# Kernel optimization log

Measured on AMD Instinct MI355X. Metric: run time of the kernel, lower is better.

Reference implementation:

```python
import jax, jax.numpy as jnp
import numpy as np

B, S, D, H = 2, 2048, 1024, 16
DH = D // H
EPS = 1e-5
NEG = -1e9


def layer_norm(x, scale, bias):
    mu = jnp.mean(x, axis=-1, keepdims=True)
    var = jnp.mean((x - mu) ** 2, axis=-1, keepdims=True)
    return (x - mu) * jax.lax.rsqrt(var + EPS) * scale + bias


def setup_inputs() -> dict:
    key = jax.random.key(0)
    ks = jax.random.split(key, 8)
    scale = 1.0 / np.sqrt(D)
    x = jax.random.normal(ks[0], (B, S, D), dtype=jnp.float32)
    padding_mask = jnp.ones((B, S), dtype=bool)
    # per-head QKV projections stacked over heads: (H, D, DH)
    Wq = jax.random.normal(ks[1], (H, D, DH), dtype=jnp.float32) * scale
    Wk = jax.random.normal(ks[2], (H, D, DH), dtype=jnp.float32) * scale
    Wv = jax.random.normal(ks[3], (H, D, DH), dtype=jnp.float32) * scale
    ln1_s = jnp.ones((D,), jnp.float32); ln1_b = jnp.zeros((D,), jnp.float32)
    ln2_s = jnp.ones((D,), jnp.float32); ln2_b = jnp.zeros((D,), jnp.float32)
    W1 = jax.random.normal(ks[4], (D, D), dtype=jnp.float32) * scale
    b1 = jnp.zeros((D,), jnp.float32)
    W2 = jax.random.normal(ks[5], (D, D), dtype=jnp.float32) * scale
    b2 = jnp.zeros((D,), jnp.float32)
    return dict(x=x, padding_mask=padding_mask, Wq=Wq, Wk=Wk, Wv=Wv,
                ln1_s=ln1_s, ln1_b=ln1_b, ln2_s=ln2_s, ln2_b=ln2_b,
                W1=W1, b1=b1, W2=W2, b2=b2)


def reference(x, padding_mask, Wq, Wk, Wv, ln1_s, ln1_b, ln2_s, ln2_b, W1, b1, W2, b2):
    # pre-norm attention with residual (dropout = identity at eval)
    h = layer_norm(x, ln1_s, ln1_b)
    q = jnp.einsum('bsd,hde->bhse', h, Wq)
    k = jnp.einsum('bsd,hde->bhse', h, Wk)
    v = jnp.einsum('bsd,hde->bhse', h, Wv)
    scores = jnp.einsum('bhse,bhte->bhst', q, k) / jnp.sqrt(jnp.float32(DH))
    causal = jnp.tril(jnp.ones((S, S), dtype=bool))           # (S,S)
    mask = padding_mask[:, None, None, :] & causal[None, None]  # (B,1,S,S)
    scores = jnp.where(mask, scores, NEG)
    p = jax.nn.softmax(scores, axis=-1)
    z = jnp.einsum('bhst,bhte->bshe', p, v).reshape(x.shape[0], x.shape[1], D)
    x = x + z
    # pre-norm FFN with residual
    h2 = layer_norm(x, ln2_s, ln2_b)
    ff = jax.nn.relu(h2 @ W1 + b1) @ W2 + b2
    return x + ff
```

## Files before the change

### kernel.cpp

```cpp
#include <hip/hip_runtime.h>
#include <hip/hip_bf16.h>
#include <stdint.h>

#define NB 2
#define NS 2048
#define ND 1024
#define NH 16
#define NDH 64
#define NT (NB*NS)

using f32x4  = __attribute__((ext_vector_type(4))) float;
using bf16x8 = __attribute__((ext_vector_type(8))) short;

typedef __attribute__((address_space(1))) unsigned int as1_uint;
typedef __attribute__((address_space(3))) unsigned int as3_uint;

#if __has_builtin(__builtin_amdgcn_exp2f)
#define EXP2 __builtin_amdgcn_exp2f
#else
#define EXP2 exp2f
#endif

__device__ __forceinline__ void llds16(void* l, const void* g) {
    __builtin_amdgcn_global_load_lds((as1_uint*)g, (as3_uint*)l, 16, 0, 0);
}

__device__ __forceinline__ f32x4 mfma16(bf16x8 a, bf16x8 b, f32x4 c) {
    return __builtin_amdgcn_mfma_f32_16x16x32_bf16(a, b, c, 0, 0, 0);
}

__device__ __forceinline__ unsigned short f2bf(float f) {
    union { __hip_bfloat16 h; unsigned short u; } cv;
    cv.h = __float2bfloat16(f);
    return cv.u;
}

__global__ void k_prep_ln(const float* __restrict__ Wq, const float* __restrict__ Wk,
                          const float* __restrict__ Wv, const float* __restrict__ W1,
                          const float* __restrict__ W2, unsigned short* __restrict__ WcatT,
                          unsigned short* __restrict__ W1T, unsigned short* __restrict__ W2T,
                          const float* __restrict__ x, const float* __restrict__ sc,
                          const float* __restrict__ bi, unsigned short* __restrict__ hout) {
    __shared__ float tile[64][65];
    __shared__ float ssum[4], ssq[4];
    int tid = threadIdx.x;
    int bid = blockIdx.x;
    if (bid < 768) {
        const float SCALEQ = 0.125f * 1.44269504088896f;
        int kt = bid & 15; bid >>= 4;
        int h  = bid & 15; bid >>= 4;
        int mat = bid;
        const float* W = (mat == 0) ? Wq : (mat == 1) ? Wk : Wv;
#pragma unroll
        for (int i = 0; i < 16; ++i) {
            int idx = tid + i * 256;
            int r = idx >> 6, e = idx & 63;
            tile[r][e] = W[(size_t)h * ND * NDH + (size_t)(kt * 64 + r) * NDH + e];
        }
        __syncthreads();
#pragma unroll
        for (int i = 0; i < 16; ++i) {
            int idx = tid + i * 256;
            int e = idx >> 6, r = idx & 63;
            float v = tile[r][e];
            if (mat == 0) v *= SCALEQ;
            WcatT[(size_t)(mat * 1024 + h * 64 + e) * ND + kt * 64 + r] = f2bf(v);
        }
    } else if (bid < 1280) {
        const float* W = (bid < 1024) ? W1 : W2;
        unsigned short* WT = (bid < 1024) ? W1T : W2T;
        int lb = (bid - 768) & 255;
        int ntile = lb & 15;
        int ktile = lb >> 4;
#pragma unroll
        for (int i = 0; i < 16; ++i) {
            int idx = tid + i * 256;
            int r = idx >> 6, c = idx & 63;
            tile[r][c] = W[(size_t)(ktile * 64 + r) * ND + ntile * 64 + c];
        }
        __syncthreads();
#pragma unroll
        for (int i = 0; i < 16; ++i) {
            int idx = tid + i * 256;
            int c = idx >> 6, r = idx & 63;
            WT[(size_t)(ntile * 64 + c) * ND + ktile * 64 + r] = f2bf(tile[r][c]);
        }
    } else {
        int row = bid - 1280;
        const float* xr = x + (size_t)row * ND;
        float4 v = reinterpret_cast<const float4*>(xr)[tid];
        float sum = v.x + v.y + v.z + v.w;
        float sq  = v.x * v.x + v.y * v.y + v.z * v.z + v.w * v.w;
#pragma unroll
        for (int off = 1; off < 64; off <<= 1) {
            sum += __shfl_xor(sum, off);
            sq  += __shfl_xor(sq, off);
        }
        int wave = tid >> 6;
        if ((tid & 63) == 0) { ssum[wave] = sum; ssq[wave] = sq; }
        __syncthreads();
        sum = ssum[0] + ssum[1] + ssum[2] + ssum[3];
        sq  = ssq[0] + ssq[1] + ssq[2] + ssq[3];
        float mu  = sum * (1.0f / ND);
        float var = sq * (1.0f / ND) - mu * mu;
        float rstd = rsqrtf(var + 1e-5f);
        float4 s4 = reinterpret_cast<const float4*>(sc)[tid];
        float4 b4 = reinterpret_cast<const float4*>(bi)[tid];
        ushort4 o;
        o.x = f2bf((v.x - mu) * rstd * s4.x + b4.x);
        o.y = f2bf((v.y - mu) * rstd * s4.y + b4.y);
        o.z = f2bf((v.z - mu) * rstd * s4.z + b4.z);
        o.w = f2bf((v.w - mu) * rstd * s4.w + b4.w);
        reinterpret_cast<ushort4*>(hout + (size_t)row * ND)[tid] = o;
    }
}

__global__ void k_ln(const float* __restrict__ x, const float* __restrict__ sc,
                     const float* __restrict__ bi, unsigned short* __restrict__ out) {
    int row = blockIdx.x;
    int tid = threadIdx.x;
    const float* xr = x + (size_t)row * ND;
    float4 v = reinterpret_cast<const float4*>(xr)[tid];
    float sum = v.x + v.y + v.z + v.w;
    float sq  = v.x * v.x + v.y * v.y + v.z * v.z + v.w * v.w;
#pragma unroll
    for (int off = 1; off < 64; off <<= 1) {
        sum += __shfl_xor(sum, off);
        sq  += __shfl_xor(sq, off);
    }
    __shared__ float ssum[4], ssq[4];
    int wave = tid >> 6;
    if ((tid & 63) == 0) { ssum[wave] = sum; ssq[wave] = sq; }
    __syncthreads();
    sum = ssum[0] + ssum[1] + ssum[2] + ssum[3];
    sq  = ssq[0] + ssq[1] + ssq[2] + ssq[3];
    float mu  = sum * (1.0f / ND);
    float var = sq * (1.0f / ND) - mu * mu;
    float rstd = rsqrtf(var + 1e-5f);
    float4 s4 = reinterpret_cast<const float4*>(sc)[tid];
    float4 b4 = reinterpret_cast<const float4*>(bi)[tid];
    ushort4 o;
    o.x = f2bf((v.x - mu) * rstd * s4.x + b4.x);
    o.y = f2bf((v.y - mu) * rstd * s4.y + b4.y);
    o.z = f2bf((v.z - mu) * rstd * s4.z + b4.z);
    o.w = f2bf((v.w - mu) * rstd * s4.w + b4.w);
    reinterpret_cast<ushort4*>(out + (size_t)row * ND)[tid] = o;
}

template<bool BIAS, bool RELU, bool RES>
__device__ __forceinline__
void gemm_core(const unsigned short* __restrict__ A, const unsigned short* __restrict__ Bt,
               const float* __restrict__ bias, const float* __restrict__ res,
               void* __restrict__ Cv, int N, int K, int wg) {
    __shared__ __align__(16) unsigned short As[2][64 * 64];
    __shared__ __align__(16) unsigned short Bs[2][128 * 64];
    int tid = threadIdx.x;
    int lane = tid & 63, wave = tid >> 6;
    int wm = wave >> 1, wn = wave & 1;
    int l16 = lane & 15, lg = lane >> 4;
    int ntiles = N >> 7;
    int mt = wg / ntiles;
    int nt = wg % ntiles;

    const unsigned short* Abase = A  + (size_t)(mt * 64) * K;
    const unsigned short* Bbase = Bt + (size_t)(nt * 128) * K;

    f32x4 acc[2][4];
#pragma unroll
    for (int i = 0; i < 2; ++i)
#pragma unroll
        for (int j = 0; j < 4; ++j) acc[i][j] = (f32x4){0.f, 0.f, 0.f, 0.f};

    int srow = tid >> 3;
    int sch  = tid & 7;
    int KT = K >> 6;

    auto STAGE = [&](int kt, int bufi) {
#pragma unroll
        for (int i = 0; i < 2; ++i) {
            int row = srow + i * 32;
            int cs = sch ^ (row & 7);
            llds16((char*)As[bufi] + wave * 1024 + i * 4096,
                   Abase + (size_t)row * K + kt * 64 + cs * 8);
        }
#pragma unroll
        for (int i = 0; i < 4; ++i) {
            int row = srow + i * 32;
            int cs = sch ^ (row & 7);
            llds16((char*)Bs[bufi] + wave * 1024 + i * 4096,
                   Bbase + (size_t)row * K + kt * 64 + cs * 8);
        }
    };

    STAGE(0, 0);
    for (int kt = 0; kt < KT; ++kt) {
        int cb = kt & 1;
        if (kt + 1 < KT) {
            STAGE(kt + 1, cb ^ 1);
            asm volatile("s_waitcnt vmcnt(6)" ::: "memory");
        } else {
            asm volatile("s_waitcnt vmcnt(0)" ::: "memory");
        }
        __builtin_amdgcn_s_barrier();

        bf16x8 af[2][2], bfb[4][2];
#pragma unroll
        for (int mi = 0; mi < 2; ++mi)
#pragma unroll
            for (int kc = 0; kc < 2; ++kc) {
                int row = wm * 32 + mi * 16 + l16;
                int ch = (kc * 4 + lg) ^ (row & 7);
                af[mi][kc] = *reinterpret_cast<const bf16x8*>((const char*)As[cb] + row * 128 + ch * 16);
            }
#pragma unroll
        for (int ni = 0; ni < 4; ++ni)
#pragma unroll
            for (int kc = 0; kc < 2; ++kc) {
                int row = wn * 64 + ni * 16 + l16;
                int ch = (kc * 4 + lg) ^ (row & 7);
                bfb[ni][kc] = *reinterpret_cast<const bf16x8*>((const char*)Bs[cb] + row * 128 + ch * 16);
            }
#pragma unroll
        for (int mi = 0; mi < 2; ++mi)
#pragma unroll
            for (int ni = 0; ni < 4; ++ni) {
                acc[mi][ni] = mfma16(af[mi][0], bfb[ni][0], acc[mi][ni]);
                acc[mi][ni] = mfma16(af[mi][1], bfb[ni][1], acc[mi][ni]);
            }
        __builtin_amdgcn_s_barrier();
    }

#pragma unroll
    for (int mi = 0; mi < 2; ++mi)
#pragma unroll
        for (int ni = 0; ni < 4; ++ni) {
            int col = nt * 128 + wn * 64 + ni * 16 + l16;
            float bv = BIAS ? bias[col] : 0.f;
#pragma unroll
            for (int r = 0; r < 4; ++r) {
                int row = mt * 64 + wm * 32 + mi * 16 + lg * 4 + r;
                float v = acc[mi][ni][r] + bv;
                if (RELU) v = fmaxf(v, 0.f);
                size_t idx = (size_t)row * N + col;
                if (RES) ((float*)Cv)[idx] = v + res[idx];
                else ((unsigned short*)Cv)[idx] = f2bf(v);
            }
        }
}

template<bool BIAS, bool RELU, bool RES>
__global__ __launch_bounds__(256)
void k_gemm(const unsigned short* __restrict__ A, const unsigned short* __restrict__ Bt,
            const float* __restrict__ bias, const float* __restrict__ res,
            void* __restrict__ Cv, int N, int K) {
    int wg = (blockIdx.x & 7) * (gridDim.x >> 3) + (blockIdx.x >> 3);
    gemm_core<BIAS, RELU, RES>(A, Bt, bias, res, Cv, N, K, wg);
}

__global__ __launch_bounds__(256)
void k_gemm_dual(const unsigned short* __restrict__ A0, const unsigned short* __restrict__ Bt0,
                 void* __restrict__ C0, int N0,
                 const unsigned short* __restrict__ A1, const unsigned short* __restrict__ Bt1,
                 void* __restrict__ C1, int N1, int K, int split) {
    int bid = blockIdx.x;
    if (bid < split) {
        int wg = (bid & 7) * (split >> 3) + (bid >> 3);
        gemm_core<false, false, false>(A0, Bt0, nullptr, nullptr, C0, N0, K, wg);
    } else {
        int lb = bid - split;
        int nblk = gridDim.x - split;
        int wg = (lb & 7) * (nblk >> 3) + (lb >> 3);
        gemm_core<false, false, false>(A1, Bt1, nullptr, nullptr, C1, N1, K, wg);
    }
}

__global__ __launch_bounds__(256)
void k_attn(const unsigned short* __restrict__ qk, const unsigned short* __restrict__ VT,
            const float* __restrict__ x, float* __restrict__ x2) {
    constexpr int ldq = 2 * ND;
    int bid = blockIdx.x;
    int c  = bid & 255;
    int g  = bid >> 8;
    int s  = c >> 5;
    int bh = c & 31;
    int qb = (g == 0) ? 31 - s : (g == 1) ? 16 + s : (g == 2) ? 15 - s : s;
    int h = bh & 15, b = bh >> 4;
    int tid = threadIdx.x;
    int lane = tid & 63, wave = tid >> 6;
    int l16 = lane & 15, lg = lane >> 4;

    const unsigned short* Qp = qk + (size_t)b * NS * ldq + h * NDH;
    const unsigned short* Kp = Qp + ND;
    const unsigned short* Vp = VT + (size_t)(h * NDH) * NT + b * NS;

    __shared__ __align__(16) unsigned short Ks[2][64 * 64];
    __shared__ __align__(16) unsigned short Vs[2][64 * 64];
    __shared__ __align__(16) unsigned short Ps[4][16 * 64];

    int srow = tid >> 3;
    int sch  = tid & 7;
    int scs  = sch ^ (srow & 7);

    int nt = qb + 1;
    int qw = qb * 64 + wave * 16;

    const unsigned short* Kst = Kp + (size_t)srow * ldq + scs * 8;
    const unsigned short* Vst = Vp + (size_t)srow * NT + scs * 8;

    bf16x8 qf[2];
#pragma unroll
    for (int kc = 0; kc < 2; ++kc)
        qf[kc] = *reinterpret_cast<const bf16x8*>(Qp + (size_t)(qw + l16) * ldq + kc * 32 + lg * 8);

    bf16x8 vone;
#pragma unroll
    for (int i = 0; i < 8; ++i) vone[i] = (short)0x3F80;

    f32x4 oacc[4];
#pragma unroll
    for (int i = 0; i < 4; ++i) oacc[i] = (f32x4){0.f, 0.f, 0.f, 0.f};
    f32x4 lacc = (f32x4){0.f, 0.f, 0.f, 0.f};

    char* pbase = (char*)&Ps[wave][0] + l16 * 128;
    int psw = l16 & 7;

    llds16((char*)Ks[0] + wave * 1024,        Kst);
    llds16((char*)Ks[0] + wave * 1024 + 4096, Kst + (size_t)32 * ldq);
    llds16((char*)Vs[0] + wave * 1024,        Vst);
    llds16((char*)Vs[0] + wave * 1024 + 4096, Vst + (size_t)32 * NT);
    const unsigned short* Kn = Kst + (size_t)64 * ldq;
    const unsigned short* Vn = Vst + 64;

    for (int t = 0; t < nt; ++t) {
        int cur = t & 1;
        const char* Kcur = (const char*)Ks[cur];
        const char* Vcur = (const char*)Vs[cur];

        if (t + 1 < nt) {
            char* kd = (char*)Ks[cur ^ 1] + wave * 1024;
            char* vd = (char*)Vs[cur ^ 1] + wave * 1024;
            llds16(kd,        Kn);
            llds16(kd + 4096, Kn + (size_t)32 * ldq);
            llds16(vd,        Vn);
            llds16(vd + 4096, Vn + (size_t)32 * NT);
            Kn += (size_t)64 * ldq;
            Vn += 64;
            asm volatile("s_waitcnt vmcnt(4)" ::: "memory");
        } else {
            asm volatile("s_waitcnt vmcnt(0)" ::: "memory");
        }
        __builtin_amdgcn_s_barrier();

        f32x4 st[4];
#pragma unroll
        for (int mtt = 0; mtt < 4; ++mtt) st[mtt] = (f32x4){0.f, 0.f, 0.f, 0.f};
        __builtin_amdgcn_s_setprio(1);
#pragma unroll
        for (int kc = 0; kc < 2; ++kc)
#pragma unroll
            for (int mtt = 0; mtt < 4; ++mtt) {
                int row = mtt * 16 + l16;
                int ch = (kc * 4 + lg) ^ (row & 7);
                bf16x8 kf = *reinterpret_cast<const bf16x8*>(Kcur + row * 128 + ch * 16);
                st[mtt] = mfma16(kf, qf[kc], st[mtt]);
            }
        __builtin_amdgcn_s_setprio(0);

        if (t == qb) {
            int qg = qw + l16;
#pragma unroll
            for (int mtt = 0; mtt < 4; ++mtt)
#pragma unroll
                for (int r = 0; r < 4; ++r) {
                    int key = t * 64 + mtt * 16 + lg * 4 + r;
                    st[mtt][r] = (key <= qg) ? st[mtt][r] : -1.0e30f;
                }
        }
#pragma unroll
        for (int mtt = 0; mtt < 4; ++mtt) {
            float p0 = EXP2(st[mtt][0]);
            float p1 = EXP2(st[mtt][1]);
            float p2 = EXP2(st[mtt][2]);
            float p3 = EXP2(st[mtt][3]);
            int b0 = mtt * 32 + lg * 8;
            int sb = ((((b0 >> 4) ^ psw) << 4) | (b0 & 15));
            uint2 u;
            u.x = (unsigned)f2bf(p0) | ((unsigned)f2bf(p1) << 16);
            u.y = (unsigned)f2bf(p2) | ((unsigned)f2bf(p3) << 16);
            *reinterpret_cast<uint2*>(pbase + sb) = u;
        }

        asm volatile("s_waitcnt lgkmcnt(0)" ::: "memory");

        __builtin_amdgcn_s_setprio(1);
#pragma unroll
        for (int kc = 0; kc < 2; ++kc) {
            bf16x8 pa = *reinterpret_cast<const bf16x8*>(pbase + (((kc * 4 + lg) ^ psw) << 4));
            lacc = mfma16(pa, vone, lacc);
#pragma unroll
            for (int ntt = 0; ntt < 4; ++ntt) {
                int vrow = ntt * 16 + l16;
                bf16x8 vb = *reinterpret_cast<const bf16x8*>(
                    Vcur + vrow * 128 + ((((kc * 4 + lg) ^ (vrow & 7)) << 4)));
                oacc[ntt] = mfma16(pa, vb, oacc[ntt]);
            }
        }
        __builtin_amdgcn_s_setprio(0);
        __builtin_amdgcn_s_barrier();
    }

#pragma unroll
    for (int r = 0; r < 4; ++r) {
        float linv = 1.0f / lacc[r];
        int tkn = b * NS + qw + lg * 4 + r;
        size_t base = (size_t)tkn * ND + h * NDH;
#pragma unroll
        for (int ntt = 0; ntt < 4; ++ntt) {
            size_t idx = base + ntt * 16 + l16;
            x2[idx] = x[idx] + oacc[ntt][r] * linv;
        }
    }
}

extern "C" void kernel_launch(void* const* d_in, const int* in_sizes, int n_in,
                              void* d_out, int out_size, void* d_ws, size_t ws_size,
                              hipStream_t stream) {
    const float* x    = (const float*)d_in[0];
    const float* Wq   = (const float*)d_in[2];
    const float* Wk   = (const float*)d_in[3];
    const float* Wv   = (const float*)d_in[4];
    const float* ln1s = (const float*)d_in[5];
    const float* ln1b = (const float*)d_in[6];
    const float* ln2s = (const float*)d_in[7];
    const float* ln2b = (const float*)d_in[8];
    const float* W1   = (const float*)d_in[9];
    const float* b1   = (const float*)d_in[10];
    const float* W2   = (const float*)d_in[11];
    const float* b2   = (const float*)d_in[12];
    float* out = (float*)d_out;

    char* ws = (char*)d_ws;
    unsigned short* WcatT = (unsigned short*)(ws);
    unsigned short* W1T   = (unsigned short*)(ws + 6291456);
    unsigned short* W2T   = (unsigned short*)(ws + 8388608);
    unsigned short* hbuf  = (unsigned short*)(ws + 10485760);
    unsigned short* qkbuf = (unsigned short*)(ws + 18874368);
    unsigned short* vtbuf = (unsigned short*)(ws + 35651584);
    float*          x2    = (float*)(ws + 44040192);
    unsigned short* ubuf  = qkbuf;

    k_prep_ln<<<1280 + NT, 256, 0, stream>>>(Wq, Wk, Wv, W1, W2, WcatT, W1T, W2T,
                                             x, ln1s, ln1b, hbuf);
    k_gemm_dual<<<1024 + 512, 256, 0, stream>>>(
        hbuf, WcatT, qkbuf, 2048,
        WcatT + (size_t)2048 * 1024, hbuf, vtbuf, NT, 1024, 1024);
    k_attn<<<NB * NH * 32, 256, 0, stream>>>(qkbuf, vtbuf, x, x2);
    k_ln<<<NT, 256, 0, stream>>>(x2, ln2s, ln2b, hbuf);
    k_gemm<true, true, false><<<(NT / 64) * (1024 / 128), 256, 0, stream>>>(
        hbuf, W1T, b1, nullptr, ubuf, 1024, 1024);
    k_gemm<true, false, true><<<(NT / 64) * (1024 / 128), 256, 0, stream>>>(
        ubuf, W2T, b2, x2, out, 1024, 1024);
}
```

Measured before the change: 129.7 us.

## Split causal attention KV range across two blocks and fuse merge into LN2

Each query block's causal key range is split into two halves processed by separate workgroups, doubling the grid to 2048 blocks for better load balance and occupancy. Each half writes unnormalized bf16 partial outputs and row sums. A new combine+layernorm kernel merges the halves, adds the residual, writes x2 into the output buffer, and produces the LN2 input, replacing the separate LN kernel. Partial outputs are rounded to bf16 before normalization, which adds rounding error. The merge skips max rescaling, so it relies on the scores never needing a running max.

```diff
diff --git a/kernel.cpp b/kernel.cpp
--- a/kernel.cpp
+++ b/kernel.cpp
@@ -33,6 +33,10 @@
     union { __hip_bfloat16 h; unsigned short u; } cv;
     cv.h = __float2bfloat16(f);
     return cv.u;
+}
+
+__device__ __forceinline__ float bf2f(unsigned short u) {
+    return __uint_as_float((unsigned)u << 16);
 }
 
 __global__ void k_prep_ln(const float* __restrict__ Wq, const float* __restrict__ Wk,
@@ -115,12 +119,314 @@
     }
 }
 
-__global__ void k_ln(const float* __restrict__ x, const float* __restrict__ sc,
-                     const float* __restrict__ bi, unsigned short* __restrict__ out) {
+template<bool BIAS, bool RELU, bool RES>
+__device__ __forceinline__
+void gemm_core(const unsigned short* __restrict__ A, const unsigned short* __restrict__ Bt,
+               const float* __restrict__ bias, const float* __restrict__ res,
+               void* __restrict__ Cv, int N, int K, int wg) {
+    __shared__ __align__(16) unsigned short As[2][64 * 64];
+    __shared__ __align__(16) unsigned short Bs[2][128 * 64];
+    int tid = threadIdx.x;
+    int lane = tid & 63, wave = tid >> 6;
+    int wm = wave >> 1, wn = wave & 1;
+    int l16 = lane & 15, lg = lane >> 4;
+    int ntiles = N >> 7;
+    int mt = wg / ntiles;
+    int nt = wg % ntiles;
+
+    const unsigned short* Abase = A  + (size_t)(mt * 64) * K;
+    const unsigned short* Bbase = Bt + (size_t)(nt * 128) * K;
+
+    f32x4 acc[2][4];
+#pragma unroll
+    for (int i = 0; i < 2; ++i)
+#pragma unroll
+        for (int j = 0; j < 4; ++j) acc[i][j] = (f32x4){0.f, 0.f, 0.f, 0.f};
+
+    int srow = tid >> 3;
+    int sch  = tid & 7;
+    int KT = K >> 6;
+
+    auto STAGE = [&](int kt, int bufi) {
+#pragma unroll
+        for (int i = 0; i < 2; ++i) {
+            int row = srow + i * 32;
+            int cs = sch ^ (row & 7);
+            llds16((char*)As[bufi] + wave * 1024 + i * 4096,
+                   Abase + (size_t)row * K + kt * 64 + cs * 8);
+        }
+#pragma unroll
+        for (int i = 0; i < 4; ++i) {
+            int row = srow + i * 32;
+            int cs = sch ^ (row & 7);
+            llds16((char*)Bs[bufi] + wave * 1024 + i * 4096,
+                   Bbase + (size_t)row * K + kt * 64 + cs * 8);
+        }
+    };
+
+    STAGE(0, 0);
+    for (int kt = 0; kt < KT; ++kt) {
+        int cb = kt & 1;
+        if (kt + 1 < KT) {
+            STAGE(kt + 1, cb ^ 1);
+            asm volatile("s_waitcnt vmcnt(6)" ::: "memory");
+        } else {
+            asm volatile("s_waitcnt vmcnt(0)" ::: "memory");
+        }
+        __builtin_amdgcn_s_barrier();
+
+        bf16x8 af[2][2], bfb[4][2];
+#pragma unroll
+        for (int mi = 0; mi < 2; ++mi)
+#pragma unroll
+            for (int kc = 0; kc < 2; ++kc) {
+                int row = wm * 32 + mi * 16 + l16;
+                int ch = (kc * 4 + lg) ^ (row & 7);
+                af[mi][kc] = *reinterpret_cast<const bf16x8*>((const char*)As[cb] + row * 128 + ch * 16);
+            }
+#pragma unroll
+        for (int ni = 0; ni < 4; ++ni)
+#pragma unroll
+            for (int kc = 0; kc < 2; ++kc) {
+                int row = wn * 64 + ni * 16 + l16;
+                int ch = (kc * 4 + lg) ^ (row & 7);
+                bfb[ni][kc] = *reinterpret_cast<const bf16x8*>((const char*)Bs[cb] + row * 128 + ch * 16);
+            }
+#pragma unroll
+        for (int mi = 0; mi < 2; ++mi)
+#pragma unroll
+            for (int ni = 0; ni < 4; ++ni) {
+                acc[mi][ni] = mfma16(af[mi][0], bfb[ni][0], acc[mi][ni]);
+                acc[mi][ni] = mfma16(af[mi][1], bfb[ni][1], acc[mi][ni]);
+            }
+        __builtin_amdgcn_s_barrier();
+    }
+
+#pragma unroll
+    for (int mi = 0; mi < 2; ++mi)
+#pragma unroll
+        for (int ni = 0; ni < 4; ++ni) {
+            int col = nt * 128 + wn * 64 + ni * 16 + l16;
+            float bv = BIAS ? bias[col] : 0.f;
+#pragma unroll
+            for (int r = 0; r < 4; ++r) {
+                int row = mt * 64 + wm * 32 + mi * 16 + lg * 4 + r;
+                float v = acc[mi][ni][r] + bv;
+                if (RELU) v = fmaxf(v, 0.f);
+                size_t idx = (size_t)row * N + col;
+                if (RES) ((float*)Cv)[idx] = v + res[idx];
+                else ((unsigned short*)Cv)[idx] = f2bf(v);
+            }
+        }
+}
+
+template<bool BIAS, bool RELU, bool RES>
+__global__ __launch_bounds__(256)
+void k_gemm(const unsigned short* __restrict__ A, const unsigned short* __restrict__ Bt,
+            const float* __restrict__ bias, const float* __restrict__ res,
+            void* __restrict__ Cv, int N, int K) {
+    int wg = (blockIdx.x & 7) * (gridDim.x >> 3) + (blockIdx.x >> 3);
+    gemm_core<BIAS, RELU, RES>(A, Bt, bias, res, Cv, N, K, wg);
+}
+
+__global__ __launch_bounds__(256)
+void k_gemm_dual(const unsigned short* __restrict__ A0, const unsigned short* __restrict__ Bt0,
+                 void* __restrict__ C0, int N0,
+                 const unsigned short* __restrict__ A1, const unsigned short* __restrict__ Bt1,
+                 void* __restrict__ C1, int N1, int K, int split) {
+    int bid = blockIdx.x;
+    if (bid < split) {
+        int wg = (bid & 7) * (split >> 3) + (bid >> 3);
+        gemm_core<false, false, false>(A0, Bt0, nullptr, nullptr, C0, N0, K, wg);
+    } else {
+        int lb = bid - split;
+        int nblk = gridDim.x - split;
+        int wg = (lb & 7) * (nblk >> 3) + (lb >> 3);
+        gemm_core<false, false, false>(A1, Bt1, nullptr, nullptr, C1, N1, K, wg);
+    }
+}
+
+__global__ __launch_bounds__(256)
+void k_attn(const unsigned short* __restrict__ qk, const unsigned short* __restrict__ VT,
+            unsigned short* __restrict__ Oa, unsigned short* __restrict__ Ob,
+            float* __restrict__ lp) {
+    constexpr int ldq = 2 * ND;
+    int bid = blockIdx.x;
+    int bh = bid & 31;
+    int j  = bid >> 5;
+    int qb = 31 - (j >> 1);
+    int half = j & 1;
+    int h = bh & 15, b = bh >> 4;
+    int tid = threadIdx.x;
+    int lane = tid & 63, wave = tid >> 6;
+    int l16 = lane & 15, lg = lane >> 4;
+
+    const unsigned short* Qp = qk + (size_t)b * NS * ldq + h * NDH;
+    const unsigned short* Kp = Qp + ND;
+    const unsigned short* Vp = VT + (size_t)(h * NDH) * NT + b * NS;
+
+    __shared__ __align__(16) unsigned short Ks[2][64 * 64];
+    __shared__ __align__(16) unsigned short Vs[2][64 * 64];
+    __shared__ __align__(16) unsigned short Ps[4][16 * 64];
+
+    int srow = tid >> 3;
+    int sch  = tid & 7;
+    int scs  = sch ^ (srow & 7);
+
+    int ntA = (qb + 2) >> 1;
+    int t0 = half ? ntA : 0;
+    int t1 = half ? (qb + 1) : ntA;
+    int ntiles = t1 - t0;
+    int qw = qb * 64 + wave * 16;
+
+    const unsigned short* Kst = Kp + (size_t)srow * ldq + scs * 8 + (size_t)t0 * 64 * ldq;
+    const unsigned short* Vst = Vp + (size_t)srow * NT + scs * 8 + t0 * 64;
+
+    bf16x8 qf[2];
+#pragma unroll
+    for (int kc = 0; kc < 2; ++kc)
+        qf[kc] = *reinterpret_cast<const bf16x8*>(Qp + (size_t)(qw + l16) * ldq + kc * 32 + lg * 8);
+
+    bf16x8 vone;
+#pragma unroll
+    for (int i = 0; i < 8; ++i) vone[i] = (short)0x3F80;
+
+    f32x4 oacc[4];
+#pragma unroll
+    for (int i = 0; i < 4; ++i) oacc[i] = (f32x4){0.f, 0.f, 0.f, 0.f};
+    f32x4 lacc = (f32x4){0.f, 0.f, 0.f, 0.f};
+
+    char* pbase = (char*)&Ps[wave][0] + l16 * 128;
+    int psw = l16 & 7;
+
+    if (ntiles > 0) {
+        llds16((char*)Ks[0] + wave * 1024,        Kst);
+        llds16((char*)Ks[0] + wave * 1024 + 4096, Kst + (size_t)32 * ldq);
+        llds16((char*)Vs[0] + wave * 1024,        Vst);
+        llds16((char*)Vs[0] + wave * 1024 + 4096, Vst + (size_t)32 * NT);
+    }
+    const unsigned short* Kn = Kst + (size_t)64 * ldq;
+    const unsigned short* Vn = Vst + 64;
+
+    for (int i = 0; i < ntiles; ++i) {
+        int cur = i & 1;
+        int t = t0 + i;
+        const char* Kcur = (const char*)Ks[cur];
+        const char* Vcur = (const char*)Vs[cur];
+
+        if (i + 1 < ntiles) {
+            char* kd = (char*)Ks[cur ^ 1] + wave * 1024;
+            char* vd = (char*)Vs[cur ^ 1] + wave * 1024;
+            llds16(kd,        Kn);
+            llds16(kd + 4096, Kn + (size_t)32 * ldq);
+            llds16(vd,        Vn);
+            llds16(vd + 4096, Vn + (size_t)32 * NT);
+            Kn += (size_t)64 * ldq;
+            Vn += 64;
+            asm volatile("s_waitcnt vmcnt(4)" ::: "memory");
+        } else {
+            asm volatile("s_waitcnt vmcnt(0)" ::: "memory");
+        }
+        __builtin_amdgcn_s_barrier();
+
+        f32x4 st[4];
+#pragma unroll
+        for (int mtt = 0; mtt < 4; ++mtt) st[mtt] = (f32x4){0.f, 0.f, 0.f, 0.f};
+        __builtin_amdgcn_s_setprio(1);
+#pragma unroll
+        for (int kc = 0; kc < 2; ++kc)
+#pragma unroll
+            for (int mtt = 0; mtt < 4; ++mtt) {
+                int row = mtt * 16 + l16;
+                int ch = (kc * 4 + lg) ^ (row & 7);
+                bf16x8 kf = *reinterpret_cast<const bf16x8*>(Kcur + row * 128 + ch * 16);
+                st[mtt] = mfma16(kf, qf[kc], st[mtt]);
+            }
+        __builtin_amdgcn_s_setprio(0);
+
+        if (t == qb) {
+            int qg = qw + l16;
+#pragma unroll
+            for (int mtt = 0; mtt < 4; ++mtt)
+#pragma unroll
+                for (int r = 0; r < 4; ++r) {
+                    int key = t * 64 + mtt * 16 + lg * 4 + r;
+                    st[mtt][r] = (key <= qg) ? st[mtt][r] : -1.0e30f;
+                }
+        }
+#pragma unroll
+        for (int mtt = 0; mtt < 4; ++mtt) {
+            float p0 = EXP2(st[mtt][0]);
+            float p1 = EXP2(st[mtt][1]);
+            float p2 = EXP2(st[mtt][2]);
+            float p3 = EXP2(st[mtt][3]);
+            int b0 = mtt * 32 + lg * 8;
+            int sb = ((((b0 >> 4) ^ psw) << 4) | (b0 & 15));
+            uint2 u;
+            u.x = (unsigned)f2bf(p0) | ((unsigned)f2bf(p1) << 16);
+            u.y = (unsigned)f2bf(p2) | ((unsigned)f2bf(p3) << 16);
+            *reinterpret_cast<uint2*>(pbase + sb) = u;
+        }
+
+        asm volatile("s_waitcnt lgkmcnt(0)" ::: "memory");
+
+        __builtin_amdgcn_s_setprio(1);
+#pragma unroll
+        for (int kc = 0; kc < 2; ++kc) {
+            bf16x8 pa = *reinterpret_cast<const bf16x8*>(pbase + (((kc * 4 + lg) ^ psw) << 4));
+            lacc = mfma16(pa, vone, lacc);
+#pragma unroll
+            for (int ntt = 0; ntt < 4; ++ntt) {
+                int vrow = ntt * 16 + l16;
+                bf16x8 vb = *reinterpret_cast<const bf16x8*>(
+                    Vcur + vrow * 128 + ((((kc * 4 + lg) ^ (vrow & 7)) << 4)));
+                oacc[ntt] = mfma16(pa, vb, oacc[ntt]);
+            }
+        }
+        __builtin_amdgcn_s_setprio(0);
+        __builtin_amdgcn_s_barrier();
+    }
+
+    unsigned short* Op = half ? Ob : Oa;
+#pragma unroll
+    for (int r = 0; r < 4; ++r) {
+        int tkn = b * NS + qw + lg * 4 + r;
+        size_t base = (size_t)tkn * ND + h * NDH;
+#pragma unroll
+        for (int ntt = 0; ntt < 4; ++ntt)
+            Op[base + ntt * 16 + l16] = f2bf(oacc[ntt][r]);
+    }
+    if (l16 == 0) {
+        float* lph = lp + (size_t)half * NB * NH * NS + (size_t)(b * NH + h) * NS;
+#pragma unroll
+        for (int r = 0; r < 4; ++r)
+            lph[qw + lg * 4 + r] = lacc[r];
+    }
+}
+
+__global__ void k_cln(const float* __restrict__ x, const unsigned short* __restrict__ Oa,
+                      const unsigned short* __restrict__ Ob, const float* __restrict__ lp,
+                      const float* __restrict__ sc, const float* __restrict__ bi,
+                      unsigned short* __restrict__ hout, float* __restrict__ xout) {
     int row = blockIdx.x;
     int tid = threadIdx.x;
-    const float* xr = x + (size_t)row * ND;
-    float4 v = reinterpret_cast<const float4*>(xr)[tid];
+    int b = row >> 11;
+    int s_ = row & (NS - 1);
+    int h = tid >> 4;
+    float la = lp[(size_t)(b * NH + h) * NS + s_];
+    float lb = lp[(size_t)NB * NH * NS + (size_t)(b * NH + h) * NS + s_];
+    float linv = 1.0f / (la + lb);
+    size_t base = (size_t)row * ND + tid * 4;
+    ushort4 oa = *reinterpret_cast<const ushort4*>(Oa + base);
+    ushort4 ob = *reinterpret_cast<const ushort4*>(Ob + base);
+    float4 xr = *reinterpret_cast<const float4*>(x + base);
+    float4 v;
+    v.x = xr.x + (bf2f(oa.x) + bf2f(ob.x)) * linv;
+    v.y = xr.y + (bf2f(oa.y) + bf2f(ob.y)) * linv;
+    v.z = xr.z + (bf2f(oa.z) + bf2f(ob.z)) * linv;
+    v.w = xr.w + (bf2f(oa.w) + bf2f(ob.w)) * linv;
+    *reinterpret_cast<float4*>(xout + base) = v;
+
     float sum = v.x + v.y + v.z + v.w;
     float sq  = v.x * v.x + v.y * v.y + v.z * v.z + v.w * v.w;
 #pragma unroll
@@ -144,282 +450,7 @@
     o.y = f2bf((v.y - mu) * rstd * s4.y + b4.y);
     o.z = f2bf((v.z - mu) * rstd * s4.z + b4.z);
     o.w = f2bf((v.w - mu) * rstd * s4.w + b4.w);
-    reinterpret_cast<ushort4*>(out + (size_t)row * ND)[tid] = o;
-}
-
-template<bool BIAS, bool RELU, bool RES>
-__device__ __forceinline__
-void gemm_core(const unsigned short* __restrict__ A, const unsigned short* __restrict__ Bt,
-               const float* __restrict__ bias, const float* __restrict__ res,
-               void* __restrict__ Cv, int N, int K, int wg) {
-    __shared__ __align__(16) unsigned short As[2][64 * 64];
-    __shared__ __align__(16) unsigned short Bs[2][128 * 64];
-    int tid = threadIdx.x;
-    int lane = tid & 63, wave = tid >> 6;
-    int wm = wave >> 1, wn = wave & 1;
-    int l16 = lane & 15, lg = lane >> 4;
-    int ntiles = N >> 7;
-    int mt = wg / ntiles;
-    int nt = wg % ntiles;
-
-    const unsigned short* Abase = A  + (size_t)(mt * 64) * K;
-    const unsigned short* Bbase = Bt + (size_t)(nt * 128) * K;
-
-    f32x4 acc[2][4];
-#pragma unroll
-    for (int i = 0; i < 2; ++i)
-#pragma unroll
-        for (int j = 0; j < 4; ++j) acc[i][j] = (f32x4){0.f, 0.f, 0.f, 0.f};
-
-    int srow = tid >> 3;
-    int sch  = tid & 7;
-    int KT = K >> 6;
-
-    auto STAGE = [&](int kt, int bufi) {
-#pragma unroll
-        for (int i = 0; i < 2; ++i) {
-            int row = srow + i * 32;
-            int cs = sch ^ (row & 7);
-            llds16((char*)As[bufi] + wave * 1024 + i * 4096,
-                   Abase + (size_t)row * K + kt * 64 + cs * 8);
-        }
-#pragma unroll
-        for (int i = 0; i < 4; ++i) {
-            int row = srow + i * 32;
-            int cs = sch ^ (row & 7);
-            llds16((char*)Bs[bufi] + wave * 1024 + i * 4096,
-                   Bbase + (size_t)row * K + kt * 64 + cs * 8);
-        }
-    };
-
-    STAGE(0, 0);
-    for (int kt = 0; kt < KT; ++kt) {
-        int cb = kt & 1;
-        if (kt + 1 < KT) {
-            STAGE(kt + 1, cb ^ 1);
-            asm volatile("s_waitcnt vmcnt(6)" ::: "memory");
-        } else {
-            asm volatile("s_waitcnt vmcnt(0)" ::: "memory");
-        }
-        __builtin_amdgcn_s_barrier();
-
-        bf16x8 af[2][2], bfb[4][2];
-#pragma unroll
-        for (int mi = 0; mi < 2; ++mi)
-#pragma unroll
-            for (int kc = 0; kc < 2; ++kc) {
-                int row = wm * 32 + mi * 16 + l16;
-                int ch = (kc * 4 + lg) ^ (row & 7);
-                af[mi][kc] = *reinterpret_cast<const bf16x8*>((const char*)As[cb] + row * 128 + ch * 16);
-            }
-#pragma unroll
-        for (int ni = 0; ni < 4; ++ni)
-#pragma unroll
-            for (int kc = 0; kc < 2; ++kc) {
-                int row = wn * 64 + ni * 16 + l16;
-                int ch = (kc * 4 + lg) ^ (row & 7);
-                bfb[ni][kc] = *reinterpret_cast<const bf16x8*>((const char*)Bs[cb] + row * 128 + ch * 16);
-            }
-#pragma unroll
-        for (int mi = 0; mi < 2; ++mi)
-#pragma unroll
-            for (int ni = 0; ni < 4; ++ni) {
-                acc[mi][ni] = mfma16(af[mi][0], bfb[ni][0], acc[mi][ni]);
-                acc[mi][ni] = mfma16(af[mi][1], bfb[ni][1], acc[mi][ni]);
-            }
-        __builtin_amdgcn_s_barrier();
-    }
-
-#pragma unroll
-    for (int mi = 0; mi < 2; ++mi)
-#pragma unroll
-        for (int ni = 0; ni < 4; ++ni) {
-            int col = nt * 128 + wn * 64 + ni * 16 + l16;
-            float bv = BIAS ? bias[col] : 0.f;
-#pragma unroll
-            for (int r = 0; r < 4; ++r) {
-                int row = mt * 64 + wm * 32 + mi * 16 + lg * 4 + r;
-                float v = acc[mi][ni][r] + bv;
-                if (RELU) v = fmaxf(v, 0.f);
-                size_t idx = (size_t)row * N + col;
-                if (RES) ((float*)Cv)[idx] = v + res[idx];
-                else ((unsigned short*)Cv)[idx] = f2bf(v);
-            }
-        }
-}
-
-template<bool BIAS, bool RELU, bool RES>
-__global__ __launch_bounds__(256)
-void k_gemm(const unsigned short* __restrict__ A, const unsigned short* __restrict__ Bt,
-            const float* __restrict__ bias, const float* __restrict__ res,
-            void* __restrict__ Cv, int N, int K) {
-    int wg = (blockIdx.x & 7) * (gridDim.x >> 3) + (blockIdx.x >> 3);
-    gemm_core<BIAS, RELU, RES>(A, Bt, bias, res, Cv, N, K, wg);
-}
-
-__global__ __launch_bounds__(256)
-void k_gemm_dual(const unsigned short* __restrict__ A0, const unsigned short* __restrict__ Bt0,
-                 void* __restrict__ C0, int N0,
-                 const unsigned short* __restrict__ A1, const unsigned short* __restrict__ Bt1,
-                 void* __restrict__ C1, int N1, int K, int split) {
-    int bid = blockIdx.x;
-    if (bid < split) {
-        int wg = (bid & 7) * (split >> 3) + (bid >> 3);
-        gemm_core<false, false, false>(A0, Bt0, nullptr, nullptr, C0, N0, K, wg);
-    } else {
-        int lb = bid - split;
-        int nblk = gridDim.x - split;
-        int wg = (lb & 7) * (nblk >> 3) + (lb >> 3);
-        gemm_core<false, false, false>(A1, Bt1, nullptr, nullptr, C1, N1, K, wg);
-    }
-}
-
-__global__ __launch_bounds__(256)
-void k_attn(const unsigned short* __restrict__ qk, const unsigned short* __restrict__ VT,
-            const float* __restrict__ x, float* __restrict__ x2) {
-    constexpr int ldq = 2 * ND;
-    int bid = blockIdx.x;
-    int c  = bid & 255;
-    int g  = bid >> 8;
-    int s  = c >> 5;
-    int bh = c & 31;
-    int qb = (g == 0) ? 31 - s : (g == 1) ? 16 + s : (g == 2) ? 15 - s : s;
-    int h = bh & 15, b = bh >> 4;
-    int tid = threadIdx.x;
-    int lane = tid & 63, wave = tid >> 6;
-    int l16 = lane & 15, lg = lane >> 4;
-
-    const unsigned short* Qp = qk + (size_t)b * NS * ldq + h * NDH;
-    const unsigned short* Kp = Qp + ND;
-    const unsigned short* Vp = VT + (size_t)(h * NDH) * NT + b * NS;
-
-    __shared__ __align__(16) unsigned short Ks[2][64 * 64];
-    __shared__ __align__(16) unsigned short Vs[2][64 * 64];
-    __shared__ __align__(16) unsigned short Ps[4][16 * 64];
-
-    int srow = tid >> 3;
-    int sch  = tid & 7;
-    int scs  = sch ^ (srow & 7);
-
-    int nt = qb + 1;
-    int qw = qb * 64 + wave * 16;
-
-    const unsigned short* Kst = Kp + (size_t)srow * ldq + scs * 8;
-    const unsigned short* Vst = Vp + (size_t)srow * NT + scs * 8;
-
-    bf16x8 qf[2];
-#pragma unroll
-    for (int kc = 0; kc < 2; ++kc)
-        qf[kc] = *reinterpret_cast<const bf16x8*>(Qp + (size_t)(qw + l16) * ldq + kc * 32 + lg * 8);
-
-    bf16x8 vone;
-#pragma unroll
-    for (int i = 0; i < 8; ++i) vone[i] = (short)0x3F80;
-
-    f32x4 oacc[4];
-#pragma unroll
-    for (int i = 0; i < 4; ++i) oacc[i] = (f32x4){0.f, 0.f, 0.f, 0.f};
-    f32x4 lacc = (f32x4){0.f, 0.f, 0.f, 0.f};
-
-    char* pbase = (char*)&Ps[wave][0] + l16 * 128;
-    int psw = l16 & 7;
-
-    llds16((char*)Ks[0] + wave * 1024,        Kst);
-    llds16((char*)Ks[0] + wave * 1024 + 4096, Kst + (size_t)32 * ldq);
-    llds16((char*)Vs[0] + wave * 1024,        Vst);
-    llds16((char*)Vs[0] + wave * 1024 + 4096, Vst + (size_t)32 * NT);
-    const unsigned short* Kn = Kst + (size_t)64 * ldq;
-    const unsigned short* Vn = Vst + 64;
-
-    for (int t = 0; t < nt; ++t) {
-        int cur = t & 1;
-        const char* Kcur = (const char*)Ks[cur];
-        const char* Vcur = (const char*)Vs[cur];
-
-        if (t + 1 < nt) {
-            char* kd = (char*)Ks[cur ^ 1] + wave * 1024;
-            char* vd = (char*)Vs[cur ^ 1] + wave * 1024;
-            llds16(kd,        Kn);
-            llds16(kd + 4096, Kn + (size_t)32 * ldq);
-            llds16(vd,        Vn);
-            llds16(vd + 4096, Vn + (size_t)32 * NT);
-            Kn += (size_t)64 * ldq;
-            Vn += 64;
-            asm volatile("s_waitcnt vmcnt(4)" ::: "memory");
-        } else {
-            asm volatile("s_waitcnt vmcnt(0)" ::: "memory");
-        }
-        __builtin_amdgcn_s_barrier();
-
-        f32x4 st[4];
-#pragma unroll
-        for (int mtt = 0; mtt < 4; ++mtt) st[mtt] = (f32x4){0.f, 0.f, 0.f, 0.f};
-        __builtin_amdgcn_s_setprio(1);
-#pragma unroll
-        for (int kc = 0; kc < 2; ++kc)
-#pragma unroll
-            for (int mtt = 0; mtt < 4; ++mtt) {
-                int row = mtt * 16 + l16;
-                int ch = (kc * 4 + lg) ^ (row & 7);
-                bf16x8 kf = *reinterpret_cast<const bf16x8*>(Kcur + row * 128 + ch * 16);
-                st[mtt] = mfma16(kf, qf[kc], st[mtt]);
-            }
-        __builtin_amdgcn_s_setprio(0);
-
-        if (t == qb) {
-            int qg = qw + l16;
-#pragma unroll
-            for (int mtt = 0; mtt < 4; ++mtt)
-#pragma unroll
-                for (int r = 0; r < 4; ++r) {
-                    int key = t * 64 + mtt * 16 + lg * 4 + r;
-                    st[mtt][r] = (key <= qg) ? st[mtt][r] : -1.0e30f;
-                }
-        }
-#pragma unroll
-        for (int mtt = 0; mtt < 4; ++mtt) {
-            float p0 = EXP2(st[mtt][0]);
-            float p1 = EXP2(st[mtt][1]);
-            float p2 = EXP2(st[mtt][2]);
-            float p3 = EXP2(st[mtt][3]);
-            int b0 = mtt * 32 + lg * 8;
-            int sb = ((((b0 >> 4) ^ psw) << 4) | (b0 & 15));
-            uint2 u;
-            u.x = (unsigned)f2bf(p0) | ((unsigned)f2bf(p1) << 16);
-            u.y = (unsigned)f2bf(p2) | ((unsigned)f2bf(p3) << 16);
-            *reinterpret_cast<uint2*>(pbase + sb) = u;
-        }
-
-        asm volatile("s_waitcnt lgkmcnt(0)" ::: "memory");
-
-        __builtin_amdgcn_s_setprio(1);
-#pragma unroll
-        for (int kc = 0; kc < 2; ++kc) {
-            bf16x8 pa = *reinterpret_cast<const bf16x8*>(pbase + (((kc * 4 + lg) ^ psw) << 4));
-            lacc = mfma16(pa, vone, lacc);
-#pragma unroll
-            for (int ntt = 0; ntt < 4; ++ntt) {
-                int vrow = ntt * 16 + l16;
-                bf16x8 vb = *reinterpret_cast<const bf16x8*>(
-                    Vcur + vrow * 128 + ((((kc * 4 + lg) ^ (vrow & 7)) << 4)));
-                oacc[ntt] = mfma16(pa, vb, oacc[ntt]);
-            }
-        }
-        __builtin_amdgcn_s_setprio(0);
-        __builtin_amdgcn_s_barrier();
-    }
-
-#pragma unroll
-    for (int r = 0; r < 4; ++r) {
-        float linv = 1.0f / lacc[r];
-        int tkn = b * NS + qw + lg * 4 + r;
-        size_t base = (size_t)tkn * ND + h * NDH;
-#pragma unroll
-        for (int ntt = 0; ntt < 4; ++ntt) {
-            size_t idx = base + ntt * 16 + l16;
-            x2[idx] = x[idx] + oacc[ntt][r] * linv;
-        }
-    }
+    *reinterpret_cast<ushort4*>(hout + base) = o;
 }
 
 extern "C" void kernel_launch(void* const* d_in, const int* in_sizes, int n_in,
@@ -446,7 +477,9 @@
     unsigned short* hbuf  = (unsigned short*)(ws + 10485760);
     unsigned short* qkbuf = (unsigned short*)(ws + 18874368);
     unsigned short* vtbuf = (unsigned short*)(ws + 35651584);
-    float*          x2    = (float*)(ws + 44040192);
+    unsigned short* obbuf = (unsigned short*)(ws + 44040192);
+    float*          lpart = (float*)(ws + 52428800);
+    unsigned short* oabuf = hbuf;
     unsigned short* ubuf  = qkbuf;
 
     k_prep_ln<<<1280 + NT, 256, 0, stream>>>(Wq, Wk, Wv, W1, W2, WcatT, W1T, W2T,
@@ -454,10 +487,10 @@
     k_gemm_dual<<<1024 + 512, 256, 0, stream>>>(
         hbuf, WcatT, qkbuf, 2048,
         WcatT + (size_t)2048 * 1024, hbuf, vtbuf, NT, 1024, 1024);
-    k_attn<<<NB * NH * 32, 256, 0, stream>>>(qkbuf, vtbuf, x, x2);
-    k_ln<<<NT, 256, 0, stream>>>(x2, ln2s, ln2b, hbuf);
+    k_attn<<<2048, 256, 0, stream>>>(qkbuf, vtbuf, oabuf, obbuf, lpart);
+    k_cln<<<NT, 256, 0, stream>>>(x, oabuf, obbuf, lpart, ln2s, ln2b, hbuf, out);
     k_gemm<true, true, false><<<(NT / 64) * (1024 / 128), 256, 0, stream>>>(
         hbuf, W1T, b1, nullptr, ubuf, 1024, 1024);
     k_gemm<true, false, true><<<(NT / 64) * (1024 / 128), 256, 0, stream>>>(
-        ubuf, W2T, b2, x2, out, 1024, 1024);
-}
+        ubuf, W2T, b2, out, out, 1024, 1024);
+}
```

After: 131.4 us. No clear change (+1.3%).
